# Kernel tuning notes

Hardware: AMD Instinct MI355X
Metric: run time of the kernel (lower is better)

The kernel has to match this reference:

```python
import jax, jax.numpy as jnp
import numpy as np

B, S, D, H = 4, 2048, 512, 8
DK = D // H


def setup_inputs() -> dict:
    key = jax.random.key(0)
    k1, k2, k3, k4 = jax.random.split(key, 4)
    return {
        "Zq": jax.random.normal(k1, (B, S, D), dtype=jnp.float32),
        "Zkv": jax.random.normal(k2, (B, S, D), dtype=jnp.float32),
        "mask": jnp.zeros((1, 1, S, S), dtype=jnp.float32),
        "Wqkv": jax.random.normal(k3, (D, 3 * D), dtype=jnp.float32),
        "Wout": jax.random.normal(k4, (D, D), dtype=jnp.float32),
    }


def reference(Zq, Zkv, mask, Wqkv, Wout):
    d_k = Wqkv.shape[0] // H
    Wq, Wk, Wv = jnp.split(Wqkv, 3, axis=-1)
    b, s, d = Zq.shape
    # project and split heads: [B,S,D] -> [B,H,S,dk]
    Q = (Zq @ Wq).reshape(b, s, H, d_k).transpose(0, 2, 1, 3)
    K = (Zkv @ Wk).reshape(b, s, H, d_k).transpose(0, 2, 1, 3)
    V = (Zkv @ Wv).reshape(b, s, H, d_k).transpose(0, 2, 1, 3)
    scale = d_k ** -0.5
    scores = jnp.einsum("bhqd,bhkd->bhqk", Q, K) * scale + mask
    attn = jax.nn.softmax(scores, axis=-1)  # [B,H,Sq,Skv]
    ctx = jnp.einsum("bhqk,bhkd->bhqd", attn, V)
    out = ctx.transpose(0, 2, 1, 3).reshape(b, s, d) @ Wout
    return out, attn.mean(axis=1)
```

## Files before the change

### kernel.cpp

```cpp
#include <hip/hip_runtime.h>
#include <cstdint>

#define B_ 4
#define S_ 2048
#define D_ 512
#define H_ 8
#define DK_ 64
#define SCALE 0.125f
#define KSTR 84
#define PSTR 68

using bfrag = __attribute__((ext_vector_type(8))) __bf16;
using b4    = __attribute__((ext_vector_type(4))) __bf16;
using f4    = __attribute__((ext_vector_type(4))) float;
using f16v  = __attribute__((ext_vector_type(16))) float;

#define MFMA16(a, b, c) __builtin_amdgcn_mfma_f32_16x16x32_bf16(a, b, c, 0, 0, 0)
#define MFMA32(a, b, c) __builtin_amdgcn_mfma_f32_32x32x16_bf16(a, b, c, 0, 0, 0)

__global__ __launch_bounds__(256) void wtr_all(
    const float* __restrict__ Wqkv, const float* __restrict__ Wout,
    __bf16* __restrict__ WqTh, __bf16* __restrict__ WqTl,
    __bf16* __restrict__ WkTh, __bf16* __restrict__ WkTl,
    __bf16* __restrict__ WvTh, __bf16* __restrict__ WoTh) {
  const int by = blockIdx.y;
  const int idx = blockIdx.x * 256 + threadIdx.x;
  const int k = idx & 511, n = idx >> 9;
  const float* W = (by == 3) ? Wout : Wqkv;
  const int ldw = (by == 3) ? 512 : 1536;
  const int c0 = (by == 3) ? 0 : by * 512;
  const float x = W[(size_t)k * ldw + c0 + n];
  const __bf16 h = (__bf16)x;
  __bf16* th = (by == 0) ? WqTh : (by == 1) ? WkTh : (by == 2) ? WvTh : WoTh;
  th[(size_t)n * 512 + k] = h;
  if (by < 2) {
    __bf16* tl = (by == 0) ? WqTl : WkTl;
    tl[(size_t)n * 512 + k] = (__bf16)(x - (float)h);
  }
}

template <bool AF32, bool BF32, bool LO, int MODE>
__global__ __launch_bounds__(256) void gemm_mfma(
    const void* __restrict__ Ap, const void* __restrict__ Bp, const void* __restrict__ Blop,
    float* __restrict__ Cf, __bf16* __restrict__ Oh, __bf16* __restrict__ Ol) {
  __shared__ __bf16 Ash[64 * 40];
  __shared__ __bf16 Asl[64 * 40];
  __shared__ __bf16 Bsh[64 * 40];
  __shared__ __bf16 Bsl[64 * 40];

  const int tid = threadIdx.x;
  const int m0 = blockIdx.y * 64, n0 = blockIdx.x * 64;
  const int row = tid >> 2, seg = tid & 3;
  const int lane = tid & 63, wv = tid >> 6;
  const int wm = (wv & 1) * 32, wn = (wv >> 1) * 32;
  const int qd = lane >> 4, ln = lane & 15;

  f4 acc[2][2];
#pragma unroll
  for (int i = 0; i < 2; i++)
#pragma unroll
    for (int j = 0; j < 2; j++)
#pragma unroll
      for (int r = 0; r < 4; r++) acc[i][j][r] = 0.f;

  for (int kt = 0; kt < 512; kt += 32) {
    const size_t abase = (size_t)(m0 + row) * 512 + kt + seg * 8;
    const size_t bbase = (size_t)(n0 + row) * 512 + kt + seg * 8;
    float4 a0, a1, b0, b1, bl0;
    if constexpr (AF32) {
      const float* A = (const float*)Ap;
      a0 = *(const float4*)&A[abase];
      a1 = *(const float4*)&A[abase + 4];
    } else {
      const __bf16* A = (const __bf16*)Ap;
      a0 = *(const float4*)&A[abase];
    }
    if constexpr (BF32) {
      const float* Bm = (const float*)Bp;
      b0 = *(const float4*)&Bm[bbase];
      b1 = *(const float4*)&Bm[bbase + 4];
    } else {
      const __bf16* Bm = (const __bf16*)Bp;
      b0 = *(const float4*)&Bm[bbase];
      if constexpr (LO) {
        const __bf16* Bl = (const __bf16*)Blop;
        bl0 = *(const float4*)&Bl[bbase];
      }
    }
    __syncthreads();
    if constexpr (AF32) {
      float x[8] = {a0.x, a0.y, a0.z, a0.w, a1.x, a1.y, a1.z, a1.w};
      bfrag h, l;
#pragma unroll
      for (int j = 0; j < 8; j++) {
        h[j] = (__bf16)x[j];
        l[j] = (__bf16)(x[j] - (float)h[j]);
      }
      *(bfrag*)&Ash[row * 40 + seg * 8] = h;
      if constexpr (LO) *(bfrag*)&Asl[row * 40 + seg * 8] = l;
    } else {
      *(float4*)&Ash[row * 40 + seg * 8] = a0;
    }
    if constexpr (BF32) {
      float x[8] = {b0.x, b0.y, b0.z, b0.w, b1.x, b1.y, b1.z, b1.w};
      bfrag h;
#pragma unroll
      for (int j = 0; j < 8; j++) h[j] = (__bf16)x[j];
      *(bfrag*)&Bsh[row * 40 + seg * 8] = h;
    } else {
      *(float4*)&Bsh[row * 40 + seg * 8] = b0;
      if constexpr (LO) *(float4*)&Bsl[row * 40 + seg * 8] = bl0;
    }
    __syncthreads();

    bfrag ah[2], al[2], bh[2], bl[2];
#pragma unroll
    for (int mi = 0; mi < 2; mi++) {
      ah[mi] = *(bfrag*)&Ash[(wm + mi * 16 + ln) * 40 + qd * 8];
      if constexpr (LO) al[mi] = *(bfrag*)&Asl[(wm + mi * 16 + ln) * 40 + qd * 8];
    }
#pragma unroll
    for (int ni = 0; ni < 2; ni++) {
      bh[ni] = *(bfrag*)&Bsh[(wn + ni * 16 + ln) * 40 + qd * 8];
      if constexpr (LO) bl[ni] = *(bfrag*)&Bsl[(wn + ni * 16 + ln) * 40 + qd * 8];
    }
#pragma unroll
    for (int mi = 0; mi < 2; mi++)
#pragma unroll
      for (int ni = 0; ni < 2; ni++) {
        acc[mi][ni] = MFMA16(ah[mi], bh[ni], acc[mi][ni]);
        if constexpr (LO) {
          acc[mi][ni] = MFMA16(ah[mi], bl[ni], acc[mi][ni]);
          acc[mi][ni] = MFMA16(al[mi], bh[ni], acc[mi][ni]);
        }
      }
  }

#pragma unroll
  for (int mi = 0; mi < 2; mi++)
#pragma unroll
    for (int ni = 0; ni < 2; ni++)
#pragma unroll
      for (int r = 0; r < 4; r++) {
        const int mrow = m0 + wm + mi * 16 + qd * 4 + r;
        const int ncol = n0 + wn + ni * 16 + ln;
        const float c = acc[mi][ni][r];
        if constexpr (MODE == 0) {
          Cf[(size_t)mrow * 512 + ncol] = c;
        } else if constexpr (MODE == 1) {
          const int b = mrow >> 11, s = mrow & (S_ - 1);
          const int h = ncol >> 6, dk = ncol & 63;
          const size_t o = (((size_t)b * H_ + h) * S_ + s) * DK_ + dk;
          __bf16 hh = (__bf16)c;
          Oh[o] = hh;
          Ol[o] = (__bf16)(c - (float)hh);
        } else {
          const int h = mrow >> 6, dk = mrow & 63;
          const int b = ncol >> 11, s = ncol & (S_ - 1);
          Oh[(((size_t)b * H_ + h) * DK_ + dk) * S_ + s] = (__bf16)c;
        }
      }
}

__global__ __launch_bounds__(256) void attn_fctx(
    const __bf16* __restrict__ Qh_, const __bf16* __restrict__ Ql_,
    const __bf16* __restrict__ Kh_, const __bf16* __restrict__ Kl_,
    const __bf16* __restrict__ VT, const float* __restrict__ mask,
    __bf16* __restrict__ CTXb, float* __restrict__ MR, float* __restrict__ LR,
    __bf16* __restrict__ E, float* __restrict__ MT) {
  __shared__ __bf16 Ksh[64 * KSTR];
  __shared__ __bf16 Ksl[64 * KSTR];
  __shared__ __bf16 Vs[64 * KSTR];
  __shared__ __bf16 Ps[128 * PSTR];
  __shared__ float als[128];
  const int tid = threadIdx.x, lane = tid & 63, wv = tid >> 6;
  const int l31 = lane & 31, kh = lane >> 5;
  const int qd = lane >> 4, ln = lane & 15;
  const int bh = blockIdx.y;
  const int q0b = blockIdx.x * 128;
  const int q0w = q0b + wv * 32;
  const int srow = tid >> 2, sseg = tid & 3;

  bfrag qhf[4], qlf[4];
#pragma unroll
  for (int ks = 0; ks < 4; ks++) {
    const size_t qb = ((size_t)bh * S_ + q0w + l31) * DK_ + ks * 16 + kh * 8;
    qhf[ks] = *(const bfrag*)&Qh_[qb];
    qlf[ks] = *(const bfrag*)&Ql_[qb];
  }

  float m = -3.0e38f, l = 0.f;
  f4 cacc[2][4];
#pragma unroll
  for (int mt = 0; mt < 2; mt++)
#pragma unroll
    for (int nt = 0; nt < 4; nt++)
#pragma unroll
      for (int r = 0; r < 4; r++) cacc[mt][nt][r] = 0.f;

  float4 h0, h1, l0, l1, v0, v1;
  {
    const size_t kb = ((size_t)bh * S_ + srow) * DK_ + sseg * 16;
    const size_t vb = ((size_t)bh * DK_ + srow) * S_ + sseg * 16;
    h0 = *(const float4*)&Kh_[kb]; h1 = *(const float4*)&Kh_[kb + 8];
    l0 = *(const float4*)&Kl_[kb]; l1 = *(const float4*)&Kl_[kb + 8];
    v0 = *(const float4*)&VT[vb];  v1 = *(const float4*)&VT[vb + 8];
  }

  for (int kt = 0; kt < S_; kt += 64) {
    __syncthreads();
    *(float4*)&Ksh[srow * KSTR + sseg * 16] = h0;
    *(float4*)&Ksh[srow * KSTR + sseg * 16 + 8] = h1;
    *(float4*)&Ksl[srow * KSTR + sseg * 16] = l0;
    *(float4*)&Ksl[srow * KSTR + sseg * 16 + 8] = l1;
    *(float4*)&Vs[srow * KSTR + sseg * 16] = v0;
    *(float4*)&Vs[srow * KSTR + sseg * 16 + 8] = v1;
    __syncthreads();

    f4 mk[2][4];
#pragma unroll
    for (int t = 0; t < 2; t++)
#pragma unroll
      for (int g = 0; g < 4; g++)
        mk[t][g] = *(const f4*)&mask[(size_t)(q0w + l31) * S_ + kt + t * 32 + g * 8 + 4 * kh];

    if (kt + 64 < S_) {
      const size_t kb = ((size_t)bh * S_ + kt + 64 + srow) * DK_ + sseg * 16;
      const size_t vb = ((size_t)bh * DK_ + srow) * S_ + kt + 64 + sseg * 16;
      h0 = *(const float4*)&Kh_[kb]; h1 = *(const float4*)&Kh_[kb + 8];
      l0 = *(const float4*)&Kl_[kb]; l1 = *(const float4*)&Kl_[kb + 8];
      v0 = *(const float4*)&VT[vb];  v1 = *(const float4*)&VT[vb + 8];
    }

    f16v z[2];
#pragma unroll
    for (int t = 0; t < 2; t++)
#pragma unroll
      for (int r = 0; r < 16; r++) z[t][r] = 0.f;
#pragma unroll
    for (int t = 0; t < 2; t++)
#pragma unroll
      for (int ks = 0; ks < 4; ks++) {
        bfrag kbh = *(bfrag*)&Ksh[(t * 32 + l31) * KSTR + ks * 16 + kh * 8];
        bfrag kbl = *(bfrag*)&Ksl[(t * 32 + l31) * KSTR + ks * 16 + kh * 8];
        z[t] = MFMA32(kbh, qhf[ks], z[t]);
        z[t] = MFMA32(kbl, qhf[ks], z[t]);
        z[t] = MFMA32(kbh, qlf[ks], z[t]);
      }

#pragma unroll
    for (int t = 0; t < 2; t++)
#pragma unroll
      for (int r = 0; r < 16; r++)
        z[t][r] = fmaf(z[t][r], SCALE, mk[t][r >> 2][r & 3]);

    float tm = z[0][0];
#pragma unroll
    for (int t = 0; t < 2; t++)
#pragma unroll
      for (int r = 0; r < 16; r++) tm = fmaxf(tm, z[t][r]);
    tm = fmaxf(tm, __shfl_xor(tm, 32, 64));
    const float nm = fmaxf(m, tm);
    const float al = __expf(m - nm);
    m = nm;
    if (lane < 32) als[wv * 32 + lane] = al;

    float ls = 0.f;
#pragma unroll
    for (int t = 0; t < 2; t++)
#pragma unroll
      for (int g = 0; g < 4; g++) {
        const float e0 = __expf(z[t][g * 4 + 0] - nm);
        const float e1 = __expf(z[t][g * 4 + 1] - nm);
        const float e2 = __expf(z[t][g * 4 + 2] - nm);
        const float e3 = __expf(z[t][g * 4 + 3] - nm);
        ls += (e0 + e1) + (e2 + e3);
        b4 pk;
        pk[0] = (__bf16)e0; pk[1] = (__bf16)e1;
        pk[2] = (__bf16)e2; pk[3] = (__bf16)e3;
        *(b4*)&Ps[(wv * 32 + l31) * PSTR + t * 32 + g * 8 + 4 * kh] = pk;
      }
    l = l * al + ls;

    if (lane < 32)
      MT[((size_t)bh * 32 + (kt >> 6)) * S_ + q0w + lane] = m;

#pragma unroll
    for (int mt = 0; mt < 2; mt++) {
      f4 av = *(f4*)&als[wv * 32 + mt * 16 + qd * 4];
#pragma unroll
      for (int nt = 0; nt < 4; nt++)
#pragma unroll
        for (int r = 0; r < 4; r++) cacc[mt][nt][r] *= av[r];
    }

    bfrag pa[2][2];
#pragma unroll
    for (int mt = 0; mt < 2; mt++)
#pragma unroll
      for (int ks = 0; ks < 2; ks++)
        pa[mt][ks] = *(bfrag*)&Ps[(wv * 32 + mt * 16 + ln) * PSTR + ks * 32 + qd * 8];
#pragma unroll
    for (int nt = 0; nt < 4; nt++)
#pragma unroll
      for (int ks = 0; ks < 2; ks++) {
        bfrag vbf = *(bfrag*)&Vs[(nt * 16 + ln) * KSTR + ks * 32 + qd * 8];
#pragma unroll
        for (int mt = 0; mt < 2; mt++)
          cacc[mt][nt] = MFMA16(pa[mt][ks], vbf, cacc[mt][nt]);
      }

#pragma unroll
    for (int c = 0; c < 4; c++) {
      const int row = wv * 32 + (lane >> 3) + c * 8;
      const int ch = lane & 7;
      f4 ev = *(f4*)&Ps[row * PSTR + ch * 8];
      __builtin_nontemporal_store(
          ev, (f4*)&E[((size_t)bh * S_ + q0b + row) * S_ + kt + ch * 8]);
    }
  }

  l += __shfl_xor(l, 32, 64);
  if (lane < 32) {
    MR[(size_t)bh * S_ + q0w + lane] = m;
    LR[(size_t)bh * S_ + q0w + lane] = l;
    als[wv * 32 + lane] = 1.0f / l;
  }
  const int b = bh >> 3, h = bh & 7;
#pragma unroll
  for (int mt = 0; mt < 2; mt++) {
    f4 iv = *(f4*)&als[wv * 32 + mt * 16 + qd * 4];
#pragma unroll
    for (int nt = 0; nt < 4; nt++)
#pragma unroll
      for (int r = 0; r < 4; r++)
        CTXb[((size_t)b * S_ + q0w + mt * 16 + qd * 4 + r) * D_ + h * DK_ + nt * 16 + ln] =
            (__bf16)(cacc[mt][nt][r] * iv[r]);
  }
}

__global__ __launch_bounds__(256) void mean_rescale(
    const __bf16* __restrict__ E, const float* __restrict__ MT,
    const float* __restrict__ MR, const float* __restrict__ LR,
    float* __restrict__ meanout) {
  const int t = threadIdx.x;
  const int qr = t >> 3, seg = t & 7;
  const int b = blockIdx.y, ks = blockIdx.z;
  const int qg = blockIdx.x * 32 + qr;

  float mf[H_], il[H_];
#pragma unroll
  for (int h = 0; h < H_; h++) {
    const int bh = b * H_ + h;
    mf[h] = MR[(size_t)bh * S_ + qg];
    il[h] = 1.0f / LR[(size_t)bh * S_ + qg];
  }

  for (int kc = 0; kc < 8; kc++) {
    const int k0 = ks * 512 + kc * 64;
    const int tk = k0 >> 6;
    float acc[8];
#pragma unroll
    for (int j = 0; j < 8; j++) acc[j] = 0.f;
#pragma unroll
    for (int h = 0; h < H_; h++) {
      const int bh = b * H_ + h;
      const float mt = MT[((size_t)bh * 32 + tk) * S_ + qg];
      const float sc = __expf(mt - mf[h]) * il[h];
      bfrag e = __builtin_nontemporal_load(
          (const bfrag*)&E[((size_t)bh * S_ + qg) * S_ + k0 + seg * 8]);
#pragma unroll
      for (int j = 0; j < 8; j++) acc[j] += (float)e[j] * sc;
    }
    f4 o0, o1;
    o0[0] = acc[0] * 0.125f; o0[1] = acc[1] * 0.125f;
    o0[2] = acc[2] * 0.125f; o0[3] = acc[3] * 0.125f;
    o1[0] = acc[4] * 0.125f; o1[1] = acc[5] * 0.125f;
    o1[2] = acc[6] * 0.125f; o1[3] = acc[7] * 0.125f;
    float* mp = &meanout[((size_t)b * S_ + qg) * S_ + k0 + seg * 8];
    *(f4*)&mp[0] = o0;
    *(f4*)&mp[4] = o1;
  }
}

extern "C" void kernel_launch(void* const* d_in, const int* in_sizes, int n_in,
                              void* d_out, int out_size, void* d_ws, size_t ws_size,
                              hipStream_t stream) {
  (void)in_sizes; (void)n_in; (void)out_size; (void)ws_size;
  const float* Zq = (const float*)d_in[0];
  const float* Zkv = (const float*)d_in[1];
  const float* mask = (const float*)d_in[2];
  const float* Wqkv = (const float*)d_in[3];
  const float* Wout = (const float*)d_in[4];

  float* out = (float*)d_out;
  float* mean = out + (size_t)B_ * S_ * D_;

  char* w = (char*)d_ws;
  const size_t WSZ = 512 * 512 * sizeof(__bf16);
  const size_t QSZ = (size_t)B_ * H_ * S_ * DK_ * sizeof(__bf16);
  __bf16* WqTh = (__bf16*)w; w += WSZ;
  __bf16* WqTl = (__bf16*)w; w += WSZ;
  __bf16* WkTh = (__bf16*)w; w += WSZ;
  __bf16* WkTl = (__bf16*)w; w += WSZ;
  __bf16* WvTh = (__bf16*)w; w += WSZ;
  __bf16* WoTh = (__bf16*)w; w += WSZ;
  __bf16* Qh = (__bf16*)w; w += QSZ;
  __bf16* Ql = (__bf16*)w; w += QSZ;
  __bf16* Kh = (__bf16*)w; w += QSZ;
  __bf16* Kl = (__bf16*)w; w += QSZ;
  __bf16* VTh = (__bf16*)w; w += QSZ;
  __bf16* CTXb = (__bf16*)w; w += QSZ;
  float* MR = (float*)w; w += (size_t)B_ * H_ * S_ * sizeof(float);
  float* LR = (float*)w; w += (size_t)B_ * H_ * S_ * sizeof(float);
  float* MT = (float*)w; w += (size_t)B_ * H_ * 32 * S_ * sizeof(float);
  __bf16* E = (__bf16*)w; w += (size_t)B_ * H_ * S_ * S_ * sizeof(__bf16);

  wtr_all<<<dim3(1024, 4), 256, 0, stream>>>(Wqkv, Wout, WqTh, WqTl, WkTh, WkTl, WvTh, WoTh);

  gemm_mfma<true, false, true, 1><<<dim3(8, 128), 256, 0, stream>>>(
      Zq, WqTh, WqTl, nullptr, Qh, Ql);
  gemm_mfma<true, false, true, 1><<<dim3(8, 128), 256, 0, stream>>>(
      Zkv, WkTh, WkTl, nullptr, Kh, Kl);
  gemm_mfma<false, true, false, 2><<<dim3(128, 8), 256, 0, stream>>>(
      WvTh, Zkv, nullptr, nullptr, VTh, nullptr);

  attn_fctx<<<dim3(16, 32), 256, 0, stream>>>(Qh, Ql, Kh, Kl, VTh, mask, CTXb, MR, LR, E, MT);
  mean_rescale<<<dim3(64, 4, 4), 256, 0, stream>>>(E, MT, MR, LR, mean);

  gemm_mfma<false, false, false, 0><<<dim3(8, 128), 256, 0, stream>>>(
      CTXb, WoTh, nullptr, out, nullptr, nullptr);
}
```

Measured before the change: 384.6 us.

## Split attention KV range across two blocks and merge partial contexts

The attention kernel's KV loop is split into two halves along a new grid z dimension, doubling the number of blocks from 512 to 1024 so more CUs are kept busy. Each half writes an unnormalized partial context plus its running max and sum into scratch space carved from the mean output buffer. A new ctx_combine kernel merges the two partials with log-sum-exp rescaling and produces the normalized context and the final row max and sum. This adds an extra launch and extra partial-context traffic, and relies on the per-tile E and MT data still being consistent with the combined max and sum used by mean_rescale.

```diff
diff --git a/kernel.cpp b/kernel.cpp
--- a/kernel.cpp
+++ b/kernel.cpp
@@ -166,7 +166,7 @@
     const __bf16* __restrict__ Qh_, const __bf16* __restrict__ Ql_,
     const __bf16* __restrict__ Kh_, const __bf16* __restrict__ Kl_,
     const __bf16* __restrict__ VT, const float* __restrict__ mask,
-    __bf16* __restrict__ CTXb, float* __restrict__ MR, float* __restrict__ LR,
+    __bf16* __restrict__ CTXp, float* __restrict__ Mp, float* __restrict__ Lp,
     __bf16* __restrict__ E, float* __restrict__ MT) {
   __shared__ __bf16 Ksh[64 * KSTR];
   __shared__ __bf16 Ksl[64 * KSTR];
@@ -180,6 +180,7 @@
   const int q0b = blockIdx.x * 128;
   const int q0w = q0b + wv * 32;
   const int srow = tid >> 2, sseg = tid & 3;
+  const int kv0 = blockIdx.z << 10;
 
   bfrag qhf[4], qlf[4];
 #pragma unroll
@@ -200,14 +201,14 @@
 
   float4 h0, h1, l0, l1, v0, v1;
   {
-    const size_t kb = ((size_t)bh * S_ + srow) * DK_ + sseg * 16;
-    const size_t vb = ((size_t)bh * DK_ + srow) * S_ + sseg * 16;
+    const size_t kb = ((size_t)bh * S_ + kv0 + srow) * DK_ + sseg * 16;
+    const size_t vb = ((size_t)bh * DK_ + srow) * S_ + kv0 + sseg * 16;
     h0 = *(const float4*)&Kh_[kb]; h1 = *(const float4*)&Kh_[kb + 8];
     l0 = *(const float4*)&Kl_[kb]; l1 = *(const float4*)&Kl_[kb + 8];
     v0 = *(const float4*)&VT[vb];  v1 = *(const float4*)&VT[vb + 8];
   }
 
-  for (int kt = 0; kt < S_; kt += 64) {
+  for (int kt = kv0; kt < kv0 + 1024; kt += 64) {
     __syncthreads();
     *(float4*)&Ksh[srow * KSTR + sseg * 16] = h0;
     *(float4*)&Ksh[srow * KSTR + sseg * 16 + 8] = h1;
@@ -224,7 +225,7 @@
       for (int g = 0; g < 4; g++)
         mk[t][g] = *(const f4*)&mask[(size_t)(q0w + l31) * S_ + kt + t * 32 + g * 8 + 4 * kh];
 
-    if (kt + 64 < S_) {
+    if (kt + 64 < kv0 + 1024) {
       const size_t kb = ((size_t)bh * S_ + kt + 64 + srow) * DK_ + sseg * 16;
       const size_t vb = ((size_t)bh * DK_ + srow) * S_ + kt + 64 + sseg * 16;
       h0 = *(const float4*)&Kh_[kb]; h1 = *(const float4*)&Kh_[kb + 8];
@@ -321,22 +322,46 @@
   }
 
   l += __shfl_xor(l, 32, 64);
+  const size_t pofs = (size_t)blockIdx.z * ((size_t)B_ * H_ * S_);
   if (lane < 32) {
-    MR[(size_t)bh * S_ + q0w + lane] = m;
-    LR[(size_t)bh * S_ + q0w + lane] = l;
-    als[wv * 32 + lane] = 1.0f / l;
-  }
+    Mp[pofs + (size_t)bh * S_ + q0w + lane] = m;
+    Lp[pofs + (size_t)bh * S_ + q0w + lane] = l;
+  }
+#pragma unroll
+  for (int mt = 0; mt < 2; mt++)
+#pragma unroll
+    for (int nt = 0; nt < 4; nt++)
+#pragma unroll
+      for (int r = 0; r < 4; r++)
+        CTXp[(pofs + (size_t)bh * S_ + q0w + mt * 16 + qd * 4 + r) * DK_ + nt * 16 + ln] =
+            (__bf16)cacc[mt][nt][r];
+}
+
+__global__ __launch_bounds__(256) void ctx_combine(
+    const __bf16* __restrict__ CTXp, const float* __restrict__ Mp,
+    const float* __restrict__ Lp, __bf16* __restrict__ CTXb,
+    float* __restrict__ MR, float* __restrict__ LR) {
+  const size_t gid = (size_t)blockIdx.x * 256 + threadIdx.x;
+  const size_t row = gid >> 4;
+  const int c4 = (int)(gid & 15) * 4;
+  const size_t NR = (size_t)B_ * H_ * S_;
+  const float m0 = Mp[row], m1 = Mp[NR + row];
+  const float l0 = Lp[row], l1 = Lp[NR + row];
+  const float m = fmaxf(m0, m1);
+  const float e0 = __expf(m0 - m), e1 = __expf(m1 - m);
+  const float lf = fmaf(l0, e0, l1 * e1);
+  const float inv = 1.0f / lf;
+  if (c4 == 0) { MR[row] = m; LR[row] = lf; }
+  const b4 a = *(const b4*)&CTXp[row * DK_ + c4];
+  const b4 bv = *(const b4*)&CTXp[(NR + row) * DK_ + c4];
+  const int bh = (int)(row >> 11);
+  const int s = (int)(row & (S_ - 1));
   const int b = bh >> 3, h = bh & 7;
-#pragma unroll
-  for (int mt = 0; mt < 2; mt++) {
-    f4 iv = *(f4*)&als[wv * 32 + mt * 16 + qd * 4];
-#pragma unroll
-    for (int nt = 0; nt < 4; nt++)
-#pragma unroll
-      for (int r = 0; r < 4; r++)
-        CTXb[((size_t)b * S_ + q0w + mt * 16 + qd * 4 + r) * D_ + h * DK_ + nt * 16 + ln] =
-            (__bf16)(cacc[mt][nt][r] * iv[r]);
-  }
+  b4 ov;
+#pragma unroll
+  for (int j = 0; j < 4; j++)
+    ov[j] = (__bf16)((((float)a[j]) * e0 + ((float)bv[j]) * e1) * inv);
+  *(b4*)&CTXb[((size_t)b * S_ + s) * D_ + h * DK_ + c4] = ov;
 }
 
 __global__ __launch_bounds__(256) void mean_rescale(
@@ -399,6 +424,7 @@
   char* w = (char*)d_ws;
   const size_t WSZ = 512 * 512 * sizeof(__bf16);
   const size_t QSZ = (size_t)B_ * H_ * S_ * DK_ * sizeof(__bf16);
+  const size_t RSZ = (size_t)B_ * H_ * S_ * sizeof(float);
   __bf16* WqTh = (__bf16*)w; w += WSZ;
   __bf16* WqTl = (__bf16*)w; w += WSZ;
   __bf16* WkTh = (__bf16*)w; w += WSZ;
@@ -411,10 +437,14 @@
   __bf16* Kl = (__bf16*)w; w += QSZ;
   __bf16* VTh = (__bf16*)w; w += QSZ;
   __bf16* CTXb = (__bf16*)w; w += QSZ;
-  float* MR = (float*)w; w += (size_t)B_ * H_ * S_ * sizeof(float);
-  float* LR = (float*)w; w += (size_t)B_ * H_ * S_ * sizeof(float);
+  float* MR = (float*)w; w += RSZ;
+  float* LR = (float*)w; w += RSZ;
   float* MT = (float*)w; w += (size_t)B_ * H_ * 32 * S_ * sizeof(float);
   __bf16* E = (__bf16*)w; w += (size_t)B_ * H_ * S_ * S_ * sizeof(__bf16);
+  char* scr = (char*)mean;
+  __bf16* CXp = (__bf16*)scr; scr += 2 * QSZ;
+  float* Mp = (float*)scr; scr += 2 * RSZ;
+  float* Lp = (float*)scr; scr += 2 * RSZ;
 
   wtr_all<<<dim3(1024, 4), 256, 0, stream>>>(Wqkv, Wout, WqTh, WqTl, WkTh, WkTl, WvTh, WoTh);
 
@@ -425,7 +455,8 @@
   gemm_mfma<false, true, false, 2><<<dim3(128, 8), 256, 0, stream>>>(
       WvTh, Zkv, nullptr, nullptr, VTh, nullptr);
 
-  attn_fctx<<<dim3(16, 32), 256, 0, stream>>>(Qh, Ql, Kh, Kl, VTh, mask, CTXb, MR, LR, E, MT);
+  attn_fctx<<<dim3(16, 32, 2), 256, 0, stream>>>(Qh, Ql, Kh, Kl, VTh, mask, CXp, Mp, Lp, E, MT);
+  ctx_combine<<<dim3(4096), 256, 0, stream>>>(CXp, Mp, Lp, CTXb, MR, LR);
   mean_rescale<<<dim3(64, 4, 4), 256, 0, stream>>>(E, MT, MR, LR, mean);
 
   gemm_mfma<false, false, false, 0><<<dim3(8, 128), 256, 0, stream>>>(
```

Result: slower. 397.4 us (+3.3%).
